# Kernel tuning notes

Measured on AMD Instinct MI355X. Metric: run time of the kernel, lower is better.

The kernel has to match this reference:

```python
import jax, jax.numpy as jnp
import numpy as np

EMBED_DIM = 2048
NUM_HEADS = 32
HEAD_DIM = EMBED_DIM // NUM_HEADS  # 64
SCALE = HEAD_DIM ** -0.5


def setup_inputs() -> dict:
    key = jax.random.key(0)
    k1, k2, k3, k4, k5 = jax.random.split(key, 5)
    B, S, D = 1, 2048, EMBED_DIM
    return {
        "hidden_states": jax.random.normal(k1, (B, S, D), jnp.float32),
        "w_qkv": jax.random.normal(k2, (3 * D, D), jnp.float32) * (D ** -0.5),
        "b_qkv": jax.random.normal(k3, (3 * D,), jnp.float32) * 0.02,
        "w_out": jax.random.normal(k4, (D, D), jnp.float32) * (D ** -0.5),
        "b_out": jax.random.normal(k5, (D,), jnp.float32) * 0.02,
    }


def reference(hidden_states, w_qkv, b_qkv, w_out, b_out):
    B, S, D = hidden_states.shape
    H, Hd = NUM_HEADS, HEAD_DIM
    # fused QKV projection: [B,S,3D]
    qkv = jnp.einsum("bsd,ed->bse", hidden_states, w_qkv) + b_qkv
    q, k, v = jnp.split(qkv, 3, axis=-1)
    # [B,H,S,Hd]
    q = q.reshape(B, S, H, Hd).transpose(0, 2, 1, 3)
    k = k.reshape(B, S, H, Hd).transpose(0, 2, 1, 3)
    v = v.reshape(B, S, H, Hd).transpose(0, 2, 1, 3)
    scores = jnp.einsum("bhqd,bhkd->bhqk", q, k) * SCALE
    causal = jnp.tril(jnp.ones((S, S), bool))  # [S,S]
    scores = jnp.where(causal, scores, jnp.finfo(scores.dtype).min)
    probs = jax.nn.softmax(scores, axis=-1)
    attn = jnp.einsum("bhqk,bhkd->bhqd", probs, v)
    attn = attn.transpose(0, 2, 1, 3).reshape(B, S, D)
    return jnp.einsum("bsd,ed->bse", attn, w_out) + b_out
```

## Files before the change

kernel.cpp:

```cpp
#include <hip/hip_runtime.h>
#include <hip/hip_bf16.h>

typedef __bf16 bf16;
typedef __attribute__((ext_vector_type(8))) __bf16 bf16x8;
typedef __attribute__((ext_vector_type(4))) float f32x4;

#define S_LEN 2048
#define DM 2048
#define NH 32
#define HD 64
#define QKV_LD 6144
#define SCALE2 0.18033688011112042f
#define DEFER_THR 8.0f

__device__ __forceinline__ float fast_exp2(float x) {
  return __builtin_amdgcn_exp2f(x);
}

__device__ __forceinline__ void gload_lds16(const bf16* g, const bf16* l) {
  __builtin_amdgcn_global_load_lds(
      (const __attribute__((address_space(1))) void*)(uintptr_t)g,
      (__attribute__((address_space(3))) void*)(uint32_t)(uintptr_t)l,
      16, 0, 0);
}

template <int CTRL>
__device__ __forceinline__ float fdpp(float x) {
  return __builtin_bit_cast(float,
      __builtin_amdgcn_update_dpp(0, __builtin_bit_cast(int, x), CTRL, 0xF, 0xF, true));
}
__device__ __forceinline__ float red16_max(float x) {
  x = fmaxf(x, fdpp<0xB1>(x));
  x = fmaxf(x, fdpp<0x4E>(x));
  x = fmaxf(x, fdpp<0x141>(x));
  x = fmaxf(x, fdpp<0x140>(x));
  return x;
}
__device__ __forceinline__ float red16_sum(float x) {
  x += fdpp<0xB1>(x);
  x += fdpp<0x4E>(x);
  x += fdpp<0x141>(x);
  x += fdpp<0x140>(x);
  return x;
}

__global__ __launch_bounds__(256) void cvt3_f32_bf16(
    const float* __restrict__ s0, bf16* __restrict__ d0, const int n0,
    const float* __restrict__ s1, bf16* __restrict__ d1, const int n1,
    const float* __restrict__ s2, bf16* __restrict__ d2, const int n2)
{
  const int total = n0 + n1 + n2;
  const int stride = gridDim.x * blockDim.x;
  for (int i = blockIdx.x * blockDim.x + threadIdx.x; i < total; i += stride) {
    const float* s; bf16* d; int j = i;
    if (j < n0)            { s = s0; d = d0; }
    else if (j - n0 < n1)  { s = s1; d = d1; j -= n0; }
    else                   { s = s2; d = d2; j -= n0 + n1; }
    const f32x4 a = *(const f32x4*)(s + (size_t)j * 8);
    const f32x4 b = *(const f32x4*)(s + (size_t)j * 8 + 4);
    bf16x8 r;
    r[0] = (bf16)a[0]; r[1] = (bf16)a[1]; r[2] = (bf16)a[2]; r[3] = (bf16)a[3];
    r[4] = (bf16)b[0]; r[5] = (bf16)b[1]; r[6] = (bf16)b[2]; r[7] = (bf16)b[3];
    *(bf16x8*)(d + (size_t)j * 8) = r;
  }
}

template <int BM, int BN, int WRN, int WCN, typename TO>
__global__ __launch_bounds__(256) void gemm_bt(
    const bf16* __restrict__ A, const bf16* __restrict__ W,
    const float* __restrict__ bias, TO* __restrict__ C,
    const int M, const int N, const int K)
{
  constexpr int WM = BM / WRN;
  constexpr int WN = BN / WCN;
  constexpr int MI = WM / 16;
  constexpr int NI = WN / 16;
  constexpr int CA = (BM * 32) / 2048;
  constexpr int CB = (BN * 32) / 2048;
  constexpr int BUF = (BM + BN) * 32;
  __shared__ __align__(16) bf16 lds[2 * BUF];
  const int tid  = threadIdx.x;
  const int lane = tid & 63;
  const int wid  = tid >> 6;
  const int wr = wid / WCN, wc = wid % WCN;
  const int row0 = blockIdx.y * BM, col0 = blockIdx.x * BN;
  const int lq = lane & 15, seg = lane >> 4;

  const f32x4 fzero = {0.f, 0.f, 0.f, 0.f};
  f32x4 acc[MI][NI];
#pragma unroll
  for (int i = 0; i < MI; ++i)
#pragma unroll
    for (int j = 0; j < NI; ++j) acc[i][j] = fzero;

  auto stage = [&](const int kt, const int b) {
    const int k0 = kt << 5;
    bf16* Ab = lds + b * BUF;
    bf16* Bb = Ab + BM * 32;
#pragma unroll
    for (int c = 0; c < CA; ++c) {
      const int idx = (c << 8) + tid;
      const int r = idx >> 2, ch = idx & 3;
      gload_lds16(A + (size_t)(row0 + r) * K + (k0 + (ch << 3)),
                  Ab + (size_t)((c << 8) + (wid << 6)) * 8);
    }
#pragma unroll
    for (int c = 0; c < CB; ++c) {
      const int idx = (c << 8) + tid;
      const int r = idx >> 2, ch = idx & 3;
      gload_lds16(W + (size_t)(col0 + r) * K + (k0 + (ch << 3)),
                  Bb + (size_t)((c << 8) + (wid << 6)) * 8);
    }
  };

  const int nk = K >> 5;
  stage(0, 0);
  __syncthreads();

  int cur = 0;
  for (int kt = 0; kt < nk; ++kt) {
    if (kt + 1 < nk) stage(kt + 1, cur ^ 1);
    const bf16* Ab = lds + cur * BUF;
    const bf16* Bb = Ab + BM * 32;
    bf16x8 af[MI], bfr[NI];
#pragma unroll
    for (int i = 0; i < MI; ++i)
      af[i]  = *(const bf16x8*)(Ab + (wr * WM + (i << 4) + lq) * 32 + seg * 8);
#pragma unroll
    for (int j = 0; j < NI; ++j)
      bfr[j] = *(const bf16x8*)(Bb + (wc * WN + (j << 4) + lq) * 32 + seg * 8);
#pragma unroll
    for (int i = 0; i < MI; ++i)
#pragma unroll
      for (int j = 0; j < NI; ++j)
        acc[i][j] = __builtin_amdgcn_mfma_f32_16x16x32_bf16(af[i], bfr[j], acc[i][j], 0, 0, 0);
    __syncthreads();
    cur ^= 1;
  }

#pragma unroll
  for (int j = 0; j < NI; ++j) {
    const int col = col0 + wc * WN + (j << 4) + lq;
    const float bv = bias[col];
#pragma unroll
    for (int i = 0; i < MI; ++i) {
      const int rbase = row0 + wr * WM + (i << 4) + (seg << 2);
#pragma unroll
      for (int r = 0; r < 4; ++r)
        C[(size_t)(rbase + r) * N + col] = (TO)(acc[i][j][r] + bv);
    }
  }
}

struct QTile {
  bf16x8 qf[2];
  f32x4  o[4];
  float  m[4], l[4];
};

__device__ __forceinline__ void qtile_init(QTile& st, const bf16* Qg,
                                           const int lq, const int seg) {
  const bf16x8 r0 = *(const bf16x8*)(Qg + (size_t)lq * QKV_LD + seg * 8);
  const bf16x8 r1 = *(const bf16x8*)(Qg + (size_t)lq * QKV_LD + 32 + seg * 8);
#pragma unroll
  for (int j = 0; j < 8; ++j) {
    st.qf[0][j] = (bf16)((float)r0[j] * SCALE2);
    st.qf[1][j] = (bf16)((float)r1[j] * SCALE2);
  }
  const f32x4 fz = {0.f, 0.f, 0.f, 0.f};
#pragma unroll
  for (int r = 0; r < 4; ++r) { st.o[r] = fz; st.m[r] = -1e30f; st.l[r] = 0.f; }
}

__device__ __forceinline__ void qtile_step(
    QTile& st, const int qb, const int nt,
    const int ws, const int lq, const int seg,
    const bf16 (&Ks)[64][64], const bf16 (&Vt)[64][64], bf16 (&Psw)[16][64])
{
  const f32x4 fz = {0.f, 0.f, 0.f, 0.f};
  f32x4 s[4];
  __builtin_amdgcn_s_setprio(1);
#pragma unroll
  for (int ct = 0; ct < 4; ++ct) {
    s[ct] = fz;
#pragma unroll
    for (int ks = 0; ks < 2; ++ks) {
      const int blk = ((ks << 2) + seg) ^ (lq & 7);
      const bf16x8 kf = *(const bf16x8*)(&Ks[(ct << 4) + lq][blk << 3]);
      s[ct] = __builtin_amdgcn_mfma_f32_16x16x32_bf16(st.qf[ks], kf, s[ct], 0, 0, 0);
    }
  }
  __builtin_amdgcn_s_setprio(0);

  if (nt == qb) {
#pragma unroll
    for (int ct = 0; ct < 4; ++ct) {
      const int key = (nt << 6) + (ct << 4) + lq;
#pragma unroll
      for (int r = 0; r < 4; ++r) {
        const int qrow = (qb << 6) + (ws << 4) + (seg << 2) + r;
        if (key > qrow) s[ct][r] = -1e30f;
      }
    }
  }

#pragma unroll
  for (int r = 0; r < 4; ++r) {
    float tm = fmaxf(fmaxf(s[0][r], s[1][r]), fmaxf(s[2][r], s[3][r]));
    tm = red16_max(tm);
    if (tm > st.m[r] + DEFER_THR) {
      const float sc = fast_exp2(st.m[r] - tm);
      st.m[r] = tm;
      st.l[r] *= sc;
#pragma unroll
      for (int dt = 0; dt < 4; ++dt) st.o[dt][r] *= sc;
    }
    float rs = 0.f;
#pragma unroll
    for (int ct = 0; ct < 4; ++ct) {
      const float p = fast_exp2(s[ct][r] - st.m[r]);
      s[ct][r] = p;
      rs += p;
    }
    rs = red16_sum(rs);
    st.l[r] += rs;
  }

#pragma unroll
  for (int ct = 0; ct < 4; ++ct)
#pragma unroll
    for (int r = 0; r < 4; ++r) {
      const int q = (seg << 2) + r;
      const int colp = ((ct << 4) + lq) ^ ((q & 7) << 3);
      Psw[q][colp] = (bf16)s[ct][r];
    }

  __builtin_amdgcn_s_setprio(1);
#pragma unroll
  for (int ks = 0; ks < 2; ++ks) {
    const int blkp = ((ks << 2) + seg) ^ (lq & 7);
    const bf16x8 af = *(const bf16x8*)(&Psw[lq][blkp << 3]);
#pragma unroll
    for (int dt = 0; dt < 4; ++dt) {
      const int xv = (lq & 7) ^ (((dt << 1) + (lq >> 3)) & 7);
      const int blkv = ((ks << 2) + seg) ^ xv;
      const bf16x8 bv = *(const bf16x8*)(&Vt[(dt << 4) + lq][blkv << 3]);
      st.o[dt] = __builtin_amdgcn_mfma_f32_16x16x32_bf16(af, bv, st.o[dt], 0, 0, 0);
    }
  }
  __builtin_amdgcn_s_setprio(0);
}

__device__ __forceinline__ void qtile_store(
    const QTile& st, bf16* __restrict__ out, const int qb, const int h,
    const int ws, const int lq, const int seg)
{
  float rinv[4];
#pragma unroll
  for (int r = 0; r < 4; ++r) rinv[r] = 1.f / st.l[r];
#pragma unroll
  for (int dt = 0; dt < 4; ++dt)
#pragma unroll
    for (int r = 0; r < 4; ++r) {
      const int qrow = (qb << 6) + (ws << 4) + (seg << 2) + r;
      out[(size_t)qrow * DM + h * HD + (dt << 4) + lq] =
          (bf16)(st.o[dt][r] * rinv[r]);
    }
}

__global__ __launch_bounds__(512) void attn_flash(
    const bf16* __restrict__ qkv, bf16* __restrict__ out)
{
  __shared__ __align__(16) bf16 Ks[64][64];
  __shared__ __align__(16) bf16 Vt[64][64];
  __shared__ __align__(16) bf16 Ps[8][16][64];
  const int qbA = blockIdx.x;
  const int qbB = 31 - qbA;
  const int h   = blockIdx.y;
  const int tid = threadIdx.x;
  const int lane = tid & 63, wid = tid >> 6;
  const int lq = lane & 15, seg = lane >> 4;
  const int myqb = (wid < 4) ? qbA : qbB;
  const int ws   = wid & 3;

  const bf16* Kg = qkv + DM + h * HD;
  const bf16* Vg = qkv + 2 * DM + h * HD;

  QTile st;
  qtile_init(st, qkv + (size_t)(myqb * 64 + ws * 16) * QKV_LD + h * HD, lq, seg);

  const int srow = tid >> 3, sch = tid & 7;

  bf16x8 kr = *(const bf16x8*)(Kg + (size_t)srow * QKV_LD + (sch << 3));
  bf16x8 vr = *(const bf16x8*)(Vg + (size_t)srow * QKV_LD + (sch << 3));

  for (int nt = 0; nt <= qbB; ++nt) {
    __syncthreads();
    *(bf16x8*)(&Ks[srow][(sch ^ (srow & 7)) << 3]) = kr;
#pragma unroll
    for (int j = 0; j < 8; ++j) {
      const int keyp = srow ^ ((j ^ sch) << 3);
      Vt[(sch << 3) + j][keyp] = vr[j];
    }
    __syncthreads();

    if (nt < qbB) {
      const int row = ((nt + 1) << 6) + srow;
      kr = *(const bf16x8*)(Kg + (size_t)row * QKV_LD + (sch << 3));
      vr = *(const bf16x8*)(Vg + (size_t)row * QKV_LD + (sch << 3));
    }

    if (nt <= myqb)
      qtile_step(st, myqb, nt, ws, lq, seg, Ks, Vt, Ps[wid]);
  }

  qtile_store(st, out, myqb, h, ws, lq, seg);
}

extern "C" void kernel_launch(void* const* d_in, const int* in_sizes, int n_in,
                              void* d_out, int out_size, void* d_ws, size_t ws_size,
                              hipStream_t stream) {
  (void)in_sizes; (void)n_in; (void)out_size; (void)ws_size;
  const float* hidden = (const float*)d_in[0];
  const float* w_qkv  = (const float*)d_in[1];
  const float* b_qkv  = (const float*)d_in[2];
  const float* w_out  = (const float*)d_in[3];
  const float* b_out  = (const float*)d_in[4];
  float* out = (float*)d_out;

  bf16* qkvbuf  = (bf16*)d_ws;
  bf16* attnbuf = qkvbuf  + (size_t)S_LEN * (3 * DM);
  bf16* hidb    = attnbuf + (size_t)S_LEN * DM;
  bf16* wqkvb   = hidb    + (size_t)S_LEN * DM;
  bf16* woutb   = wqkvb   + (size_t)(3 * DM) * DM;

  dim3 blk(256);
  cvt3_f32_bf16<<<dim3(2048), blk, 0, stream>>>(
      hidden, hidb, (S_LEN * DM) / 8,
      w_qkv, wqkvb, (3 * DM * DM) / 8,
      w_out, woutb, (DM * DM) / 8);
  gemm_bt<128, 128, 2, 2, bf16><<<dim3(48, 16), blk, 0, stream>>>(
      hidb, wqkvb, b_qkv, qkvbuf, S_LEN, 3 * DM, DM);
  attn_flash<<<dim3(16, NH), dim3(512), 0, stream>>>(qkvbuf, attnbuf);
  gemm_bt<64, 128, 1, 4, float><<<dim3(16, 32), blk, 0, stream>>>(
      attnbuf, woutb, b_out, out, S_LEN, DM, DM);
}
```

Measured before the change: 163.6 us.

## Use 256x192 tile GEMM with 512 threads for QKV projection

Adds a new GEMM kernel with 256x192 output tiles, BK=64, 8 waves, XOR-swizzled LDS, and global_load_lds double buffering, and uses it for the QKV projection. The grid drops from 768 small blocks to 256 large ones, which roughly matches the CU count and raises arithmetic intensity per tile. In exchange, each block uses about 112KB of LDS and a large accumulator set, which limits occupancy. The kernel also raises wave priority around the MFMA bursts.

```diff
diff --git a/kernel.cpp b/kernel.cpp
--- a/kernel.cpp
+++ b/kernel.cpp
@@ -62,6 +62,108 @@
     r[0] = (bf16)a[0]; r[1] = (bf16)a[1]; r[2] = (bf16)a[2]; r[3] = (bf16)a[3];
     r[4] = (bf16)b[0]; r[5] = (bf16)b[1]; r[6] = (bf16)b[2]; r[7] = (bf16)b[3];
     *(bf16x8*)(d + (size_t)j * 8) = r;
+  }
+}
+
+template <typename TO>
+__global__ __launch_bounds__(512, 2) void gemm_bt_big(
+    const bf16* __restrict__ A, const bf16* __restrict__ W,
+    const float* __restrict__ bias, TO* __restrict__ C,
+    const int M, const int N, const int K)
+{
+  constexpr int BUFE = (256 + 192) * 64;
+  __shared__ __align__(16) bf16 lds[2 * BUFE];
+  const int tid  = threadIdx.x;
+  const int lane = tid & 63;
+  const int wid  = tid >> 6;
+  const int wr = wid >> 2, wc = wid & 3;
+  const int row0 = blockIdx.y << 8;
+  const int col0 = blockIdx.x * 192;
+  const int lq = lane & 15, seg = lane >> 4;
+
+  const f32x4 fz = {0.f, 0.f, 0.f, 0.f};
+  f32x4 acc[8][3];
+#pragma unroll
+  for (int i = 0; i < 8; ++i)
+#pragma unroll
+    for (int j = 0; j < 3; ++j) acc[i][j] = fz;
+
+  auto stage = [&](const int kt, const int b) {
+    const int k0 = kt << 6;
+    bf16* Ab = lds + b * BUFE;
+    bf16* Bb = Ab + 256 * 64;
+#pragma unroll
+    for (int c = 0; c < 4; ++c) {
+      const int off16 = (c << 9) + tid;
+      const int row = off16 >> 3;
+      const int ch  = (off16 & 7) ^ (row & 7);
+      gload_lds16(A + (size_t)(row0 + row) * K + k0 + (ch << 3),
+                  Ab + (size_t)((c << 9) + (wid << 6)) * 8);
+    }
+#pragma unroll
+    for (int c = 0; c < 3; ++c) {
+      const int off16 = (c << 9) + tid;
+      const int row = off16 >> 3;
+      const int ch  = (off16 & 7) ^ (row & 7);
+      gload_lds16(W + (size_t)(col0 + row) * K + k0 + (ch << 3),
+                  Bb + (size_t)((c << 9) + (wid << 6)) * 8);
+    }
+  };
+
+  const int nt = K >> 6;
+  stage(0, 0);
+
+  for (int t = 0; t < nt; ++t) {
+    asm volatile("" ::: "memory");
+    __builtin_amdgcn_s_barrier();
+    asm volatile("" ::: "memory");
+    if (t + 1 < nt) {
+      stage(t + 1, (t + 1) & 1);
+      asm volatile("s_waitcnt vmcnt(7)" ::: "memory");
+    } else {
+      asm volatile("s_waitcnt vmcnt(0)" ::: "memory");
+    }
+    __builtin_amdgcn_s_barrier();
+    asm volatile("" ::: "memory");
+
+    const bf16* Ab = lds + (t & 1) * BUFE;
+    const bf16* Bb = Ab + 256 * 64;
+#pragma unroll
+    for (int kk = 0; kk < 2; ++kk) {
+      bf16x8 af[8], bfr[3];
+#pragma unroll
+      for (int i = 0; i < 8; ++i) {
+        const int row = (wr << 7) + (i << 4) + lq;
+        af[i] = *(const bf16x8*)(Ab + row * 64 +
+                 ((((kk << 2) + seg) ^ (row & 7)) << 3));
+      }
+#pragma unroll
+      for (int j = 0; j < 3; ++j) {
+        const int row = wc * 48 + (j << 4) + lq;
+        bfr[j] = *(const bf16x8*)(Bb + row * 64 +
+                 ((((kk << 2) + seg) ^ (row & 7)) << 3));
+      }
+      __builtin_amdgcn_s_setprio(1);
+#pragma unroll
+      for (int i = 0; i < 8; ++i)
+#pragma unroll
+        for (int j = 0; j < 3; ++j)
+          acc[i][j] = __builtin_amdgcn_mfma_f32_16x16x32_bf16(af[i], bfr[j], acc[i][j], 0, 0, 0);
+      __builtin_amdgcn_s_setprio(0);
+    }
+  }
+
+#pragma unroll
+  for (int j = 0; j < 3; ++j) {
+    const int col = col0 + wc * 48 + (j << 4) + lq;
+    const float bv = bias[col];
+#pragma unroll
+    for (int i = 0; i < 8; ++i) {
+      const int rbase = row0 + (wr << 7) + (i << 4) + (seg << 2);
+#pragma unroll
+      for (int r = 0; r < 4; ++r)
+        C[(size_t)(rbase + r) * N + col] = (TO)(acc[i][j][r] + bv);
+    }
   }
 }
 
@@ -339,7 +441,7 @@
       hidden, hidb, (S_LEN * DM) / 8,
       w_qkv, wqkvb, (3 * DM * DM) / 8,
       w_out, woutb, (DM * DM) / 8);
-  gemm_bt<128, 128, 2, 2, bf16><<<dim3(48, 16), blk, 0, stream>>>(
+  gemm_bt_big<bf16><<<dim3(32, 8), dim3(512), 0, stream>>>(
       hidb, wqkvb, b_qkv, qkvbuf, S_LEN, 3 * DM, DM);
   attn_flash<<<dim3(16, NH), dim3(512), 0, stream>>>(qkvbuf, attnbuf);
   gemm_bt<64, 128, 1, 4, float><<<dim3(16, 32), blk, 0, stream>>>(
```

Measured after the change: 155.8 us. -4.8%, faster.

## Rewrite GEMMs with BK=64 swizzled LDS, vmcnt-based pipelining and larger QKV tiles

Applied to the files above, without the earlier changes.

Replaces the GEMM kernel with a version that stages 64-wide K tiles into XOR-swizzled LDS, so fragment reads avoid bank conflicts. It waits on global-to-LDS loads with explicit vmcnt counts between raw barriers instead of a full __syncthreads. It also raises MFMA priority with setprio and gives the QKV projection 128x192 tiles with 512 threads. The aim is to cut LDS bank conflicts and barrier stalls and to improve reuse, at the cost of more LDS and registers per block and fragile hand-written wait counts.

```diff
diff --git a/kernel.cpp b/kernel.cpp
--- a/kernel.cpp
+++ b/kernel.cpp
@@ -22,6 +22,17 @@
       (const __attribute__((address_space(1))) void*)(uintptr_t)g,
       (__attribute__((address_space(3))) void*)(uint32_t)(uintptr_t)l,
       16, 0, 0);
+}
+
+template <int N>
+__device__ __forceinline__ void waitcnt_vm() {
+  if constexpr (N == 0)      asm volatile("s_waitcnt vmcnt(0)" ::: "memory");
+  else if constexpr (N == 4) asm volatile("s_waitcnt vmcnt(4)" ::: "memory");
+  else if constexpr (N == 5) asm volatile("s_waitcnt vmcnt(5)" ::: "memory");
+  else if constexpr (N == 6) asm volatile("s_waitcnt vmcnt(6)" ::: "memory");
+  else if constexpr (N == 7) asm volatile("s_waitcnt vmcnt(7)" ::: "memory");
+  else if constexpr (N == 8) asm volatile("s_waitcnt vmcnt(8)" ::: "memory");
+  else static_assert(N == 0, "add vmcnt case");
 }
 
 template <int CTRL>
@@ -65,20 +76,18 @@
   }
 }
 
-template <int BM, int BN, int WRN, int WCN, typename TO>
-__global__ __launch_bounds__(256) void gemm_bt(
+template <int BM, int BN, int WRN, int WCN, int NT, int MINW, typename TO>
+__global__ __launch_bounds__(NT, MINW) void gemm_pipe(
     const bf16* __restrict__ A, const bf16* __restrict__ W,
     const float* __restrict__ bias, TO* __restrict__ C,
     const int M, const int N, const int K)
 {
-  constexpr int WM = BM / WRN;
-  constexpr int WN = BN / WCN;
-  constexpr int MI = WM / 16;
-  constexpr int NI = WN / 16;
-  constexpr int CA = (BM * 32) / 2048;
-  constexpr int CB = (BN * 32) / 2048;
-  constexpr int BUF = (BM + BN) * 32;
-  __shared__ __align__(16) bf16 lds[2 * BUF];
+  constexpr int WM = BM / WRN, WN = BN / WCN;
+  constexpr int MI = WM / 16, NI = WN / 16;
+  constexpr int CA = (BM * 64 * 2) / (NT * 16);
+  constexpr int CB = (BN * 64 * 2) / (NT * 16);
+  constexpr int BUFE = (BM + BN) * 64;
+  __shared__ __align__(16) bf16 lds[2 * BUFE];
   const int tid  = threadIdx.x;
   const int lane = tid & 63;
   const int wid  = tid >> 6;
@@ -86,56 +95,76 @@
   const int row0 = blockIdx.y * BM, col0 = blockIdx.x * BN;
   const int lq = lane & 15, seg = lane >> 4;
 
-  const f32x4 fzero = {0.f, 0.f, 0.f, 0.f};
+  const f32x4 fz = {0.f, 0.f, 0.f, 0.f};
   f32x4 acc[MI][NI];
 #pragma unroll
   for (int i = 0; i < MI; ++i)
 #pragma unroll
-    for (int j = 0; j < NI; ++j) acc[i][j] = fzero;
+    for (int j = 0; j < NI; ++j) acc[i][j] = fz;
 
   auto stage = [&](const int kt, const int b) {
-    const int k0 = kt << 5;
-    bf16* Ab = lds + b * BUF;
-    bf16* Bb = Ab + BM * 32;
+    const int k0 = kt << 6;
+    bf16* Ab = lds + b * BUFE;
+    bf16* Bb = Ab + BM * 64;
 #pragma unroll
     for (int c = 0; c < CA; ++c) {
-      const int idx = (c << 8) + tid;
-      const int r = idx >> 2, ch = idx & 3;
-      gload_lds16(A + (size_t)(row0 + r) * K + (k0 + (ch << 3)),
-                  Ab + (size_t)((c << 8) + (wid << 6)) * 8);
+      const int off16 = c * NT + tid;
+      const int row = off16 >> 3;
+      const int ch  = (off16 & 7) ^ (row & 7);
+      gload_lds16(A + (size_t)(row0 + row) * K + k0 + (ch << 3),
+                  Ab + (size_t)(c * NT + (wid << 6)) * 8);
     }
 #pragma unroll
     for (int c = 0; c < CB; ++c) {
-      const int idx = (c << 8) + tid;
-      const int r = idx >> 2, ch = idx & 3;
-      gload_lds16(W + (size_t)(col0 + r) * K + (k0 + (ch << 3)),
-                  Bb + (size_t)((c << 8) + (wid << 6)) * 8);
+      const int off16 = c * NT + tid;
+      const int row = off16 >> 3;
+      const int ch  = (off16 & 7) ^ (row & 7);
+      gload_lds16(W + (size_t)(col0 + row) * K + k0 + (ch << 3),
+                  Bb + (size_t)(c * NT + (wid << 6)) * 8);
     }
   };
 
-  const int nk = K >> 5;
+  const int nt = K >> 6;
   stage(0, 0);
-  __syncthreads();
-
-  int cur = 0;
-  for (int kt = 0; kt < nk; ++kt) {
-    if (kt + 1 < nk) stage(kt + 1, cur ^ 1);
-    const bf16* Ab = lds + cur * BUF;
-    const bf16* Bb = Ab + BM * 32;
-    bf16x8 af[MI], bfr[NI];
-#pragma unroll
-    for (int i = 0; i < MI; ++i)
-      af[i]  = *(const bf16x8*)(Ab + (wr * WM + (i << 4) + lq) * 32 + seg * 8);
-#pragma unroll
-    for (int j = 0; j < NI; ++j)
-      bfr[j] = *(const bf16x8*)(Bb + (wc * WN + (j << 4) + lq) * 32 + seg * 8);
-#pragma unroll
-    for (int i = 0; i < MI; ++i)
-#pragma unroll
-      for (int j = 0; j < NI; ++j)
-        acc[i][j] = __builtin_amdgcn_mfma_f32_16x16x32_bf16(af[i], bfr[j], acc[i][j], 0, 0, 0);
-    __syncthreads();
-    cur ^= 1;
+
+  for (int t = 0; t < nt; ++t) {
+    asm volatile("" ::: "memory");
+    __builtin_amdgcn_s_barrier();
+    asm volatile("" ::: "memory");
+    if (t + 1 < nt) {
+      stage(t + 1, (t + 1) & 1);
+      waitcnt_vm<CA + CB>();
+    } else {
+      waitcnt_vm<0>();
+    }
+    __builtin_amdgcn_s_barrier();
+    asm volatile("" ::: "memory");
+
+    const bf16* Ab = lds + (t & 1) * BUFE;
+    const bf16* Bb = Ab + BM * 64;
+#pragma unroll
+    for (int kk = 0; kk < 2; ++kk) {
+      bf16x8 af[MI], bfr[NI];
+#pragma unroll
+      for (int i = 0; i < MI; ++i) {
+        const int row = wr * WM + (i << 4) + lq;
+        af[i] = *(const bf16x8*)(Ab + row * 64 +
+                 ((((kk << 2) + seg) ^ (row & 7)) << 3));
+      }
+#pragma unroll
+      for (int j = 0; j < NI; ++j) {
+        const int row = wc * WN + (j << 4) + lq;
+        bfr[j] = *(const bf16x8*)(Bb + row * 64 +
+                 ((((kk << 2) + seg) ^ (row & 7)) << 3));
+      }
+      __builtin_amdgcn_s_setprio(1);
+#pragma unroll
+      for (int i = 0; i < MI; ++i)
+#pragma unroll
+        for (int j = 0; j < NI; ++j)
+          acc[i][j] = __builtin_amdgcn_mfma_f32_16x16x32_bf16(af[i], bfr[j], acc[i][j], 0, 0, 0);
+      __builtin_amdgcn_s_setprio(0);
+    }
   }
 
 #pragma unroll
@@ -339,9 +368,9 @@
       hidden, hidb, (S_LEN * DM) / 8,
       w_qkv, wqkvb, (3 * DM * DM) / 8,
       w_out, woutb, (DM * DM) / 8);
-  gemm_bt<128, 128, 2, 2, bf16><<<dim3(48, 16), blk, 0, stream>>>(
+  gemm_pipe<128, 192, 2, 4, 512, 4, bf16><<<dim3(32, 16), dim3(512), 0, stream>>>(
       hidb, wqkvb, b_qkv, qkvbuf, S_LEN, 3 * DM, DM);
   attn_flash<<<dim3(16, NH), dim3(512), 0, stream>>>(qkvbuf, attnbuf);
-  gemm_bt<64, 128, 1, 4, float><<<dim3(16, 32), blk, 0, stream>>>(
+  gemm_pipe<64, 128, 1, 4, 256, 2, float><<<dim3(16, 32), dim3(256), 0, stream>>>(
       attnbuf, woutb, b_out, out, S_LEN, DM, DM);
 }
```

Measured after the change: 148.9 us. 1.1x faster.
